# Performance work log

Measured on AMD Instinct MI355X. Metric: run time of the kernel, lower is better.

## Reference

```python
import math
import jax, jax.numpy as jnp
import numpy as np

NUM_HEADS = 16
LN_EPS = 1e-5


def setup_inputs() -> dict:
    key = jax.random.key(0)
    ks = jax.random.split(key, 8)
    B, S, D = 2, 1024, 1024
    L, H = 4, NUM_HEADS
    hd = D // H
    return {
        "x": jax.random.normal(ks[0], (B, S, D), jnp.float32),
        "past_k": jax.random.normal(ks[1], (L, B, H, S, hd), jnp.float32),
        "past_v": jax.random.normal(ks[2], (L, B, H, S, hd), jnp.float32),
        "past_q": jax.random.normal(ks[3], (L, B, H, S, hd), jnp.float32),
        "Wqkv": jax.random.normal(ks[4], (3 * D, D), jnp.float32) * 0.02,
        "bqkv": jnp.zeros((3 * D,), jnp.float32),
        "Wout": jax.random.normal(ks[5], (D, D), jnp.float32) * 0.02,
        "bout": jnp.zeros((D,), jnp.float32),
    }


def reference(x, past_k, past_v, past_q, Wqkv, bqkv, Wout, bout):
    B, S, D = x.shape
    H = NUM_HEADS
    hd = D // H
    scale = 1.0 / math.sqrt(hd)

    # qkv projection + head split: [B,S,D] -> [B,H,S,hd] each
    qkv = x @ Wqkv.T + bqkv  # [B,S,3D]
    q, k, v = jnp.split(qkv, 3, axis=-1)
    split = lambda t: t.reshape(B, S, H, hd).transpose(0, 2, 1, 3)
    q, k, v = split(q), split(k), split(v)

    # causal token attention scores [B,H,S,S]
    token_scores = jnp.einsum("bhqd,bhkd->bhqk", q, k) * scale
    causal = jnp.triu(jnp.ones((S, S), bool), k=1)
    token_scores = jnp.where(causal, -jnp.inf, token_scores)

    # stack past layers: [L,B,H,S,hd] -> [B,S,L,D]
    def to_full(t):
        L = t.shape[0]
        return t.transpose(1, 3, 0, 2, 4).reshape(B, S, L, D)

    mem = jnp.concatenate([to_full(past_q), to_full(past_k), to_full(past_v)], axis=2)  # [B,S,M,D], M=3L
    M = mem.shape[2]

    # layer norm (no affine) over feature dim
    mu = mem.mean(-1, keepdims=True)
    var = mem.var(-1, keepdims=True)
    mem = (mem - mu) / jnp.sqrt(var + LN_EPS)

    # reproject through K/V slices of qkv weight
    Wk, bk = Wqkv[D:2 * D], bqkv[D:2 * D]
    Wv, bv = Wqkv[2 * D:], bqkv[2 * D:]
    rk = (mem @ Wk.T + bk).reshape(B, S, M, H, hd).transpose(0, 3, 1, 2, 4)  # [B,H,S,M,hd]
    rv = (mem @ Wv.T + bv).reshape(B, S, M, H, hd).transpose(0, 3, 1, 2, 4)

    # memory scores via per-position elementwise reduce [B,H,S,M]
    mem_scores = jnp.einsum("bhsd,bhsmd->bhsm", q, rk) * scale

    scores = jnp.concatenate([token_scores, mem_scores], axis=-1)  # [B,H,S,S+M]
    weights = jax.nn.softmax(scores, axis=-1)
    token_w, mem_w = weights[..., :S], weights[..., S:]

    token_ctx = jnp.einsum("bhqk,bhkd->bhqd", token_w, v)
    mem_ctx = jnp.einsum("bhsm,bhsmd->bhsd", mem_w, rv)
    attn = token_ctx + mem_ctx  # [B,H,S,hd]

    merged = attn.transpose(0, 2, 1, 3).reshape(B, S, D)
    out = merged @ Wout.T + bout
    return out, (k, v, q)
```

## Files before the change

### kernel.cpp

```cpp
#include <hip/hip_runtime.h>

#define BATCH 2
#define SEQ   1024
#define DIM   1024
#define NH    16
#define HD    64
#define NM    12
#define NTOK  (BATCH*SEQ)
#define MEMROWS (BATCH*SEQ*NM)
#define OUTT  2097152
#define NEGBIG (-1.0e30f)

typedef __attribute__((ext_vector_type(8))) short short8;
typedef __attribute__((ext_vector_type(4))) float f32x4;

__device__ __forceinline__ float bf2f(ushort u) {
    union { unsigned int i; float f; } t; t.i = ((unsigned int)u) << 16; return t.f;
}
__device__ __forceinline__ ushort f2bf(float f) {
    union { float f; unsigned int i; } t; t.f = f;
    unsigned int i = t.i;
    unsigned int lsb = (i >> 16) & 1u;
    i += 0x7fffu + lsb;
    return (ushort)(i >> 16);
}

__global__ __launch_bounds__(256) void cvt3_kernel(
    const float* __restrict__ a, ushort* __restrict__ ab, int na4,
    const float* __restrict__ b, ushort* __restrict__ bb, int nb4,
    const float* __restrict__ c, ushort* __restrict__ cb, int nc4)
{
    int i = blockIdx.x * 256 + threadIdx.x;
    if (i >= na4 + nb4 + nc4) return;
    const float* src; ushort* dst; int j;
    if (i < na4)            { src = a; dst = ab; j = i; }
    else if (i < na4 + nb4) { src = b; dst = bb; j = i - na4; }
    else                    { src = c; dst = cb; j = i - na4 - nb4; }
    float4 v = ((const float4*)src)[j];
    ushort4 o; o.x = f2bf(v.x); o.y = f2bf(v.y); o.z = f2bf(v.z); o.w = f2bf(v.w);
    ((ushort4*)dst)[j] = o;
}


#define QKV_BLKS 384
__global__ __launch_bounds__(256) void qkv_ln_fused_kernel(
    const ushort* __restrict__ xb, const ushort* __restrict__ Wb,
    const float* __restrict__ bias, float* __restrict__ out,
    ushort* __restrict__ qkvb,
    const float* __restrict__ pq, const float* __restrict__ pk,
    const float* __restrict__ pv, ushort* __restrict__ mem_n)
{
    const int bid = blockIdx.x;
    const int tid = threadIdx.x;
    if (bid < QKV_BLKS) {
        __shared__ ushort As[128][40];
        __shared__ ushort Bs[128][40];
        const int w = tid >> 6, lane = tid & 63;
        const int n = lane & 15, qd = lane >> 4;
        const int wr = (w >> 1) * 64, wc = (w & 1) * 64;
        const int row0 = (bid / 24) * 128, col0 = (bid % 24) * 128;
        const int r1 = tid >> 2, o1 = (tid & 3) * 8;
        const int r2 = (tid + 256) >> 2, o2 = ((tid + 256) & 3) * 8;

        f32x4 acc[4][4];
#pragma unroll
        for (int mt = 0; mt < 4; mt++)
#pragma unroll
            for (int nt = 0; nt < 4; nt++) acc[mt][nt] = (f32x4){0.f, 0.f, 0.f, 0.f};

        for (int k0 = 0; k0 < 1024; k0 += 32) {
            *(short8*)&As[r1][o1] = *(const short8*)(xb + (size_t)(row0 + r1) * 1024 + k0 + o1);
            *(short8*)&As[r2][o2] = *(const short8*)(xb + (size_t)(row0 + r2) * 1024 + k0 + o2);
            *(short8*)&Bs[r1][o1] = *(const short8*)(Wb + (size_t)(col0 + r1) * 1024 + k0 + o1);
            *(short8*)&Bs[r2][o2] = *(const short8*)(Wb + (size_t)(col0 + r2) * 1024 + k0 + o2);
            __syncthreads();
            short8 af[4], bf[4];
#pragma unroll
            for (int mt = 0; mt < 4; mt++) af[mt] = *(const short8*)&As[wr + mt * 16 + n][qd * 8];
#pragma unroll
            for (int nt = 0; nt < 4; nt++) bf[nt] = *(const short8*)&Bs[wc + nt * 16 + n][qd * 8];
#pragma unroll
            for (int mt = 0; mt < 4; mt++)
#pragma unroll
                for (int nt = 0; nt < 4; nt++)
                    acc[mt][nt] = __builtin_amdgcn_mfma_f32_16x16x32_bf16(af[mt], bf[nt], acc[mt][nt], 0, 0, 0);
            __syncthreads();
        }
#pragma unroll
        for (int mt = 0; mt < 4; mt++)
#pragma unroll
            for (int nt = 0; nt < 4; nt++)
#pragma unroll
                for (int r = 0; r < 4; r++) {
                    int row = row0 + wr + mt * 16 + qd * 4 + r;
                    int col = col0 + wc + nt * 16 + n;
                    float val = acc[mt][nt][r] + bias[col];
                    int t = col >> 10, h = (col >> 6) & 15, d = col & 63;
                    int b = row >> 10, s = row & 1023;
                    size_t idx = (((size_t)(b * NH + h) * SEQ + s) * HD) + d;
                    size_t base = (t == 0) ? (size_t)3 * OUTT : (t == 1) ? (size_t)OUTT : (size_t)2 * OUTT;
                    out[base + idx] = val;
                    qkvb[(size_t)t * OUTT + idx] = f2bf(val);
                }
    } else {
        const int wid = tid >> 6, lane = tid & 63;
        const int r = (bid - QKV_BLKS) * 4 + wid;
        const int idx = r % NM;
        const int bs = r / NM;
        const int s = bs & (SEQ - 1);
        const int b = bs >> 10;
        const int c = idx >> 2;
        const int l = idx & 3;
        const float* src = (c == 0) ? pq : ((c == 1) ? pk : pv);
        const size_t base = ((size_t)(l * BATCH + b) * NH) * (SEQ * HD) + (size_t)s * HD;

        float4 v4[4];
        float sum = 0.f, sumsq = 0.f;
#pragma unroll
        for (int p = 0; p < 4; p++) {
            int h = p * 4 + (lane >> 4);
            int d = (lane & 15) * 4;
            float4 v = *(const float4*)(src + base + (size_t)h * (SEQ * HD) + d);
            v4[p] = v;
            sum   += v.x + v.y + v.z + v.w;
            sumsq += v.x * v.x + v.y * v.y + v.z * v.z + v.w * v.w;
        }
#pragma unroll
        for (int off = 32; off > 0; off >>= 1) {
            sum   += __shfl_xor(sum, off);
            sumsq += __shfl_xor(sumsq, off);
        }
        float mu  = sum * (1.f / 1024.f);
        float var = fmaxf(sumsq * (1.f / 1024.f) - mu * mu, 0.f);
        float inv = rsqrtf(var + 1e-5f);
        ushort* dst = mem_n + (size_t)r * 1024;
#pragma unroll
        for (int p = 0; p < 4; p++) {
            int dp = (p * 64 + lane) * 4;
            ushort4 o;
            o.x = f2bf((v4[p].x - mu) * inv);
            o.y = f2bf((v4[p].y - mu) * inv);
            o.z = f2bf((v4[p].z - mu) * inv);
            o.w = f2bf((v4[p].w - mu) * inv);
            *(ushort4*)(dst + dp) = o;
        }
    }
}

__global__ __launch_bounds__(256) void mfma_out_kernel(
    const ushort* __restrict__ Ab, const ushort* __restrict__ Wb,
    const float* __restrict__ bias, float* __restrict__ C)
{
    __shared__ ushort As[128][40];
    __shared__ ushort Bs[128][40];
    const int tid = threadIdx.x;
    const int w = tid >> 6, lane = tid & 63;
    const int n = lane & 15, qd = lane >> 4;
    const int wr = (w >> 1) * 64, wc = (w & 1) * 64;
    const int row0 = blockIdx.y * 128, col0 = blockIdx.x * 128;
    const int r1 = tid >> 2, o1 = (tid & 3) * 8;
    const int r2 = (tid + 256) >> 2, o2 = ((tid + 256) & 3) * 8;

    f32x4 acc[4][4];
#pragma unroll
    for (int mt = 0; mt < 4; mt++)
#pragma unroll
        for (int nt = 0; nt < 4; nt++) acc[mt][nt] = (f32x4){0.f, 0.f, 0.f, 0.f};

    for (int k0 = 0; k0 < 1024; k0 += 32) {
        *(short8*)&As[r1][o1] = *(const short8*)(Ab + (size_t)(row0 + r1) * 1024 + k0 + o1);
        *(short8*)&As[r2][o2] = *(const short8*)(Ab + (size_t)(row0 + r2) * 1024 + k0 + o2);
        *(short8*)&Bs[r1][o1] = *(const short8*)(Wb + (size_t)(col0 + r1) * 1024 + k0 + o1);
        *(short8*)&Bs[r2][o2] = *(const short8*)(Wb + (size_t)(col0 + r2) * 1024 + k0 + o2);
        __syncthreads();
        short8 af[4], bf[4];
#pragma unroll
        for (int mt = 0; mt < 4; mt++) af[mt] = *(const short8*)&As[wr + mt * 16 + n][qd * 8];
#pragma unroll
        for (int nt = 0; nt < 4; nt++) bf[nt] = *(const short8*)&Bs[wc + nt * 16 + n][qd * 8];
#pragma unroll
        for (int mt = 0; mt < 4; mt++)
#pragma unroll
            for (int nt = 0; nt < 4; nt++)
                acc[mt][nt] = __builtin_amdgcn_mfma_f32_16x16x32_bf16(af[mt], bf[nt], acc[mt][nt], 0, 0, 0);
        __syncthreads();
    }
#pragma unroll
    for (int mt = 0; mt < 4; mt++)
#pragma unroll
        for (int nt = 0; nt < 4; nt++)
#pragma unroll
            for (int r = 0; r < 4; r++) {
                int row = row0 + wr + mt * 16 + qd * 4 + r;
                int col = col0 + wc + nt * 16 + n;
                C[(size_t)row * 1024 + col] = acc[mt][nt][r] + bias[col];
            }
}

__global__ __launch_bounds__(256) void mfma_vproj_kernel(
    const ushort* __restrict__ wvecb, const ushort* __restrict__ Wvb,
    const float* __restrict__ bv, const float* __restrict__ wmem,
    ushort* __restrict__ mergedb)
{
    __shared__ ushort As[128][40];
    __shared__ ushort Bs[64][40];
    const int tid = threadIdx.x;
    const int w = tid >> 6, lane = tid & 63;
    const int n = lane & 15, qd = lane >> 4;
    const int wr = (w >> 1) * 64, wc = (w & 1) * 32;
    const int row0 = blockIdx.x * 128;
    const int h = blockIdx.y;
    const int r1 = tid >> 2, o1 = (tid & 3) * 8;
    const int r2 = (tid + 256) >> 2, o2 = ((tid + 256) & 3) * 8;

    f32x4 acc[4][2];
#pragma unroll
    for (int mt = 0; mt < 4; mt++)
#pragma unroll
        for (int nt = 0; nt < 2; nt++) acc[mt][nt] = (f32x4){0.f, 0.f, 0.f, 0.f};

    for (int k0 = 0; k0 < 1024; k0 += 32) {
        *(short8*)&As[r1][o1] = *(const short8*)(wvecb + ((size_t)(row0 + r1) * NH + h) * 1024 + k0 + o1);
        *(short8*)&As[r2][o2] = *(const short8*)(wvecb + ((size_t)(row0 + r2) * NH + h) * 1024 + k0 + o2);
        *(short8*)&Bs[r1 & 63][o1] = *(const short8*)(Wvb + (size_t)(h * HD + (r1 & 63)) * 1024 + k0 + o1);
        __syncthreads();
        short8 af[4], bf[2];
#pragma unroll
        for (int mt = 0; mt < 4; mt++) af[mt] = *(const short8*)&As[wr + mt * 16 + n][qd * 8];
#pragma unroll
        for (int nt = 0; nt < 2; nt++) bf[nt] = *(const short8*)&Bs[wc + nt * 16 + n][qd * 8];
#pragma unroll
        for (int mt = 0; mt < 4; mt++)
#pragma unroll
            for (int nt = 0; nt < 2; nt++)
                acc[mt][nt] = __builtin_amdgcn_mfma_f32_16x16x32_bf16(af[mt], bf[nt], acc[mt][nt], 0, 0, 0);
        __syncthreads();
    }
#pragma unroll
    for (int mt = 0; mt < 4; mt++)
#pragma unroll
        for (int nt = 0; nt < 2; nt++)
#pragma unroll
            for (int r = 0; r < 4; r++) {
                int token = row0 + wr + mt * 16 + qd * 4 + r;
                int d = wc + nt * 16 + n;
                float ws = wmem[((size_t)token * NH + h) * 16 + 12];
                size_t mi = (size_t)token * DIM + h * HD + d;
                float val = bf2f(mergedb[mi]) + acc[mt][nt][r] + ws * bv[h * HD + d];
                mergedb[mi] = f2bf(val);
            }
}

#define MSC_T 8
__global__ __launch_bounds__(256) void msc_direct_kernel(
    const ushort* __restrict__ qkvb, const ushort* __restrict__ mem_n,
    const ushort* __restrict__ Wkb, const float* __restrict__ bqkv,
    float* __restrict__ msc)
{
    __shared__ ushort qs[MSC_T][16][72];
    __shared__ ushort memc[MSC_T][12][72];
    __shared__ ushort qpc[MSC_T][16][72];
    __shared__ ushort wks[4][64][72];
    __shared__ float  qbkL[MSC_T][16];

    const int tid = threadIdx.x;
    const int w = tid >> 6, lane = tid & 63;
    const int n = lane & 15, qd = lane >> 4;
    const int t0 = blockIdx.x * MSC_T;

    {
        const int rid = tid >> 1, half = tid & 1;
        const int t = rid >> 4, h = rid & 15;
        const int g = t0 + t, b = g >> 10, s = g & 1023;
        const ushort* src = qkvb + (((size_t)(b * NH + h) * SEQ + s) * HD) + half * 32;
        *(short8*)&qs[t][h][half * 32]      = *(const short8*)(src);
        *(short8*)&qs[t][h][half * 32 + 8]  = *(const short8*)(src + 8);
        *(short8*)&qs[t][h][half * 32 + 16] = *(const short8*)(src + 16);
        *(short8*)&qs[t][h][half * 32 + 24] = *(const short8*)(src + 24);
    }
    __syncthreads();
    if (tid < 128) {
        const int t = tid >> 4, h = tid & 15;
        const float* bk = bqkv + DIM + h * HD;
        float s = 0.f;
#pragma unroll
        for (int d = 0; d < HD; d++) s += bf2f(qs[t][h][d]) * bk[d];
        qbkL[t][h] = s;
    }

    f32x4 acc[2];
    acc[0] = (f32x4){0.f, 0.f, 0.f, 0.f};
    acc[1] = (f32x4){0.f, 0.f, 0.f, 0.f};

    for (int ch = 0; ch < 16; ch++) {
        const int c0 = ch * 64;
        __syncthreads();
#pragma unroll
        for (int i = 0; i < 3; i++) {
            int sid = i * 256 + tid;
            int row = sid >> 3, o8 = (sid & 7) * 8;
            int t = row / 12, m = row % 12;
            *(short8*)&memc[t][m][o8] =
                *(const short8*)(mem_n + ((size_t)(t0 + t) * NM + m) * 1024 + c0 + o8);
        }
#pragma unroll
        for (int hh = 0; hh < 4; hh++) {
            const int h = w * 4 + hh;
            const ushort* wsrc = Wkb + (size_t)(h * HD + lane) * 1024 + c0;
#pragma unroll
            for (int j = 0; j < 4; j++) {
                ushort t16[16];
                *(short8*)&t16[0] = *(const short8*)(wsrc + j * 16);
                *(short8*)&t16[8] = *(const short8*)(wsrc + j * 16 + 8);
#pragma unroll
                for (int c = 0; c < 16; c++) wks[w][j * 16 + c][lane] = t16[c];
            }
            short8 af0 = *(const short8*)&qs[n & 7][h][qd * 8];
            short8 af1 = *(const short8*)&qs[n & 7][h][32 + qd * 8];
#pragma unroll
            for (int nt = 0; nt < 4; nt++) {
                short8 bf0 = *(const short8*)&wks[w][nt * 16 + n][qd * 8];
                short8 bf1 = *(const short8*)&wks[w][nt * 16 + n][32 + qd * 8];
                f32x4 z = (f32x4){0.f, 0.f, 0.f, 0.f};
                z = __builtin_amdgcn_mfma_f32_16x16x32_bf16(af0, bf0, z, 0, 0, 0);
                z = __builtin_amdgcn_mfma_f32_16x16x32_bf16(af1, bf1, z, 0, 0, 0);
                if (qd < 2) {
#pragma unroll
                    for (int r = 0; r < 4; r++)
                        qpc[qd * 4 + r][h][nt * 16 + n] = f2bf(z[r]);
                }
            }
        }
        __syncthreads();
#pragma unroll
        for (int p = 0; p < 2; p++) {
            const int tw = w + p * 4;
            const int mrow = (n < NM) ? n : 0;
            short8 af0 = *(const short8*)&qpc[tw][n][qd * 8];
            short8 af1 = *(const short8*)&qpc[tw][n][32 + qd * 8];
            short8 bf0 = *(const short8*)&memc[tw][mrow][qd * 8];
            short8 bf1 = *(const short8*)&memc[tw][mrow][32 + qd * 8];
            acc[p] = __builtin_amdgcn_mfma_f32_16x16x32_bf16(af0, bf0, acc[p], 0, 0, 0);
            acc[p] = __builtin_amdgcn_mfma_f32_16x16x32_bf16(af1, bf1, acc[p], 0, 0, 0);
        }
    }
    if (n < NM) {
#pragma unroll
        for (int p = 0; p < 2; p++) {
            const int tw = w + p * 4;
            const size_t gt = t0 + tw;
#pragma unroll
            for (int r = 0; r < 4; r++) {
                int h = qd * 4 + r;
                msc[(gt * NH + h) * NM + n] = 0.125f * (acc[p][r] + qbkL[tw][h]);
            }
        }
    }
}

#define TQ 64
#define TK 64
__global__ __launch_bounds__(512) void flash_attn_kernel(
    const ushort* __restrict__ qkvb, const float* __restrict__ msc,
    ushort* __restrict__ mergedb, float* __restrict__ wmem)
{
    __shared__ __align__(16) char smem[55296];
    ushort (*Ks)[TK][72]  = (ushort (*)[TK][72])smem;
    ushort (*Vt)[HD][72]  = (ushort (*)[HD][72])(smem + 18432);
    ushort (*Ps)[16][72]  = (ushort (*)[16][72])(smem + 36864);
    float  (*cbuf)[64][25] = (float (*)[64][25])smem;

    const int bxr = blockIdx.x;
    const int qt = (bxr & 1) ? (bxr >> 1) : (15 - (bxr >> 1));
    const int bh = blockIdx.y;
    const int b = bh >> 4, h = bh & 15;
    const int tid = threadIdx.x;
    const int w = tid >> 6;
    const int g = w >> 2;
    const int wq = w & 3;
    const int lane = tid & 63;
    const int n = lane & 15;
    const int qd = lane >> 4;

    const ushort* qb = qkvb;
    const ushort* kb = qkvb + (size_t)OUTT;
    const ushort* vb = qkvb + (size_t)2 * OUTT;
    const size_t headoff = (size_t)bh * SEQ * HD;

    const int qrow0 = qt * TQ + wq * 16;
    const ushort* qp = qb + headoff + (size_t)(qrow0 + n) * HD;
    short8 qf0 = *(const short8*)(qp + qd * 8);
    short8 qf1 = *(const short8*)(qp + 32 + qd * 8);

    float mrow[4], lrow[4];
    f32x4 Oacc[4];
#pragma unroll
    for (int r = 0; r < 4; r++) { mrow[r] = NEGBIG; lrow[r] = 0.f; }
#pragma unroll
    for (int nt = 0; nt < 4; nt++) Oacc[nt] = (f32x4){0.f, 0.f, 0.f, 0.f};

    const int gtid = tid & 255;
    const int key = gtid >> 2;
    const int c0 = (gtid & 3) * 16;
    const int nsteps = (qt + 2) >> 1;

    for (int step = 0; step < nsteps; ++step) {
        const int kt = 2 * step + g;
        const bool act = (kt <= qt);
        if (act) {
            const ushort* kg = kb + headoff + (size_t)(kt * TK + key) * HD + c0;
            *(short8*)&Ks[g][key][c0]     = *(const short8*)kg;
            *(short8*)&Ks[g][key][c0 + 8] = *(const short8*)(kg + 8);
            const ushort* vg = vb + headoff + (size_t)(kt * TK + key) * HD + c0;
            ushort vs[16];
            *(short8*)&vs[0] = *(const short8*)vg;
            *(short8*)&vs[8] = *(const short8*)(vg + 8);
#pragma unroll
            for (int i = 0; i < 16; i++) Vt[g][c0 + i][key] = vs[i];
        }
        __syncthreads();
        if (act) {
            f32x4 sacc[4];
#pragma unroll
            for (int kc = 0; kc < 4; kc++) {
                short8 kf0 = *(const short8*)&Ks[g][kc * 16 + n][qd * 8];
                short8 kf1 = *(const short8*)&Ks[g][kc * 16 + n][32 + qd * 8];
                f32x4 z = (f32x4){0.f, 0.f, 0.f, 0.f};
                z = __builtin_amdgcn_mfma_f32_16x16x32_bf16(qf0, kf0, z, 0, 0, 0);
                z = __builtin_amdgcn_mfma_f32_16x16x32_bf16(qf1, kf1, z, 0, 0, 0);
                sacc[kc] = z;
            }
            const bool diag = (kt == qt);
#pragma unroll
            for (int kc = 0; kc < 4; kc++) {
#pragma unroll
                for (int r = 0; r < 4; r++) {
                    float sv = sacc[kc][r] * 0.125f;
                    if (diag) {
                        int qrow = qrow0 + qd * 4 + r;
                        int kk = kt * TK + kc * 16 + n;
                        if (kk > qrow) sv = NEGBIG;
                    }
                    sacc[kc][r] = sv;
                }
            }
            float alpha[4];
#pragma unroll
            for (int r = 0; r < 4; r++) {
                float mx = fmaxf(fmaxf(sacc[0][r], sacc[1][r]), fmaxf(sacc[2][r], sacc[3][r]));
                mx = fmaxf(mx, __shfl_xor(mx, 1));
                mx = fmaxf(mx, __shfl_xor(mx, 2));
                mx = fmaxf(mx, __shfl_xor(mx, 4));
                mx = fmaxf(mx, __shfl_xor(mx, 8));
                float mnew = fmaxf(mrow[r], mx);
                alpha[r] = __expf(mrow[r] - mnew);
                mrow[r] = mnew;
            }
            float psum[4] = {0.f, 0.f, 0.f, 0.f};
#pragma unroll
            for (int kc = 0; kc < 4; kc++) {
#pragma unroll
                for (int r = 0; r < 4; r++) {
                    float p = __expf(sacc[kc][r] - mrow[r]);
                    psum[r] += p;
                    Ps[w][qd * 4 + r][kc * 16 + n] = f2bf(p);
                }
            }
#pragma unroll
            for (int r = 0; r < 4; r++) {
                float ps = psum[r];
                ps += __shfl_xor(ps, 1);
                ps += __shfl_xor(ps, 2);
                ps += __shfl_xor(ps, 4);
                ps += __shfl_xor(ps, 8);
                lrow[r] = alpha[r] * lrow[r] + ps;
            }
#pragma unroll
            for (int nt = 0; nt < 4; nt++)
#pragma unroll
                for (int r = 0; r < 4; r++)
                    Oacc[nt][r] *= alpha[r];
            short8 pf0 = *(const short8*)&Ps[w][n][qd * 8];
            short8 pf1 = *(const short8*)&Ps[w][n][32 + qd * 8];
#pragma unroll
            for (int nt = 0; nt < 4; nt++) {
                short8 vf0 = *(const short8*)&Vt[g][nt * 16 + n][qd * 8];
                short8 vf1 = *(const short8*)&Vt[g][nt * 16 + n][32 + qd * 8];
                f32x4 z = Oacc[nt];
                z = __builtin_amdgcn_mfma_f32_16x16x32_bf16(pf0, vf0, z, 0, 0, 0);
                z = __builtin_amdgcn_mfma_f32_16x16x32_bf16(pf1, vf1, z, 0, 0, 0);
                Oacc[nt] = z;
            }
        }
        __syncthreads();
    }

    if (g == 1) {
        float* cb = cbuf[wq][lane];
#pragma unroll
        for (int nt = 0; nt < 4; nt++)
#pragma unroll
            for (int r = 0; r < 4; r++) cb[nt * 4 + r] = Oacc[nt][r];
#pragma unroll
        for (int r = 0; r < 4; r++) { cb[16 + r] = mrow[r]; cb[20 + r] = lrow[r]; }
    }
    __syncthreads();
    if (g == 1) return;

    {
        const float* cb = cbuf[wq][lane];
#pragma unroll
        for (int r = 0; r < 4; r++) {
            float m1 = cb[16 + r], l1 = cb[20 + r];
            float mnew = fmaxf(mrow[r], m1);
            float a0 = __expf(mrow[r] - mnew);
            float a1 = __expf(m1 - mnew);
            lrow[r] = a0 * lrow[r] + a1 * l1;
#pragma unroll
            for (int nt = 0; nt < 4; nt++)
                Oacc[nt][r] = a0 * Oacc[nt][r] + a1 * cb[nt * 4 + r];
            mrow[r] = mnew;
        }
    }

#pragma unroll
    for (int r = 0; r < 4; r++) {
        int srow = qrow0 + qd * 4 + r;
        const float* mp = msc + ((size_t)(b * SEQ + srow) * NH + h) * NM;
        float mm = NEGBIG;
#pragma unroll
        for (int j = 0; j < NM; j++) mm = fmaxf(mm, mp[j]);
        float mf = fmaxf(mrow[r], mm);
        float al = __expf(mrow[r] - mf);
        float msum = 0.f;
#pragma unroll
        for (int j = 0; j < NM; j++) msum += __expf(mp[j] - mf);
        float lf = al * lrow[r] + msum;
        float inv = 1.f / lf;
        float scale = al * inv;
        ushort* mrow_out = mergedb + (size_t)(b * SEQ + srow) * DIM + h * HD;
#pragma unroll
        for (int nt = 0; nt < 4; nt++)
            mrow_out[nt * 16 + n] = f2bf(Oacc[nt][r] * scale);
        size_t wb = ((size_t)(b * SEQ + srow) * NH + h) * 16;
        if (n < 12)       wmem[wb + n]  = __expf(mp[n] - mf) * inv;
        else if (n == 12) wmem[wb + 12] = msum * inv;
    }
}

__global__ __launch_bounds__(256) void wvec_kernel(
    const float* __restrict__ wmem, const ushort* __restrict__ mem_n,
    ushort* __restrict__ wvecb)
{
    __shared__ ushort memL[NM][1032];
    __shared__ float wL[NH][NM];
    const int bs = blockIdx.x;
    const int tid = threadIdx.x;

    for (int t = tid; t < NM * 256; t += 256) {
        int m = t >> 8, c4 = (t & 255) << 2;
        *(ushort4*)&memL[m][c4] = *(const ushort4*)(mem_n + ((size_t)bs * NM + m) * 1024 + c4);
    }
    if (tid < NH * NM) {
        int h = tid / NM, m = tid % NM;
        wL[h][m] = wmem[((size_t)bs * NH + h) * 16 + m];
    }
    __syncthreads();

    for (int h = 0; h < NH; h++) {
#pragma unroll
        for (int c0 = 0; c0 < 1024; c0 += 256) {
            int c = c0 + tid;
            float acc = 0.f;
#pragma unroll
            for (int m = 0; m < NM; m++)
                acc = fmaf(wL[h][m], bf2f(memL[m][c]), acc);
            wvecb[((size_t)bs * NH + h) * 1024 + c] = f2bf(acc);
        }
    }
}

extern "C" void kernel_launch(void* const* d_in, const int* in_sizes, int n_in,
                              void* d_out, int out_size, void* d_ws, size_t ws_size,
                              hipStream_t stream) {
    const float* x    = (const float*)d_in[0];
    const float* pk   = (const float*)d_in[1];
    const float* pv   = (const float*)d_in[2];
    const float* pq   = (const float*)d_in[3];
    const float* Wqkv = (const float*)d_in[4];
    const float* bqkv = (const float*)d_in[5];
    const float* Wout = (const float*)d_in[6];
    const float* bout = (const float*)d_in[7];
    float* out = (float*)d_out;

    ushort* mem_n  = (ushort*)d_ws;
    ushort* wvecb  = mem_n + (size_t)MEMROWS * 1024;
    float*  msc    = (float*)(wvecb + (size_t)NTOK * NH * 1024);
    float*  wmem   = msc + (size_t)NTOK * NH * NM;
    ushort* qkvb   = (ushort*)(wmem + (size_t)NTOK * NH * 16);
    ushort* Wqkvb  = qkvb + (size_t)3 * OUTT;
    ushort* Woutb  = Wqkvb + (size_t)3072 * 1024;
    ushort* xb     = Woutb + (size_t)1024 * 1024;
    ushort* mergedb = xb;

    const int na4 = NTOK * DIM / 4, nb4 = 3 * DIM * DIM / 4, nc4 = DIM * DIM / 4;

    cvt3_kernel<<<(na4 + nb4 + nc4 + 255) / 256, 256, 0, stream>>>(
        x, xb, na4, Wqkv, Wqkvb, nb4, Wout, Woutb, nc4);
    qkv_ln_fused_kernel<<<QKV_BLKS + MEMROWS / 4, 256, 0, stream>>>(
        xb, Wqkvb, bqkv, out, qkvb, pq, pk, pv, mem_n);
    msc_direct_kernel<<<NTOK / MSC_T, 256, 0, stream>>>(
        qkvb, mem_n, Wqkvb + (size_t)DIM * DIM, bqkv, msc);
    flash_attn_kernel<<<dim3(16, 32), 512, 0, stream>>>(qkvb, msc, mergedb, wmem);
    wvec_kernel<<<NTOK, 256, 0, stream>>>(wmem, mem_n, wvecb);
    mfma_vproj_kernel<<<dim3(16, NH), 256, 0, stream>>>(
        wvecb, Wqkvb + (size_t)2 * DIM * DIM, bqkv + 2 * DIM, wmem, mergedb);
    mfma_out_kernel<<<dim3(8, 16), 256, 0, stream>>>(mergedb, Woutb, bout, out);
}
```

Measured before the change: 398.6 us.

## Split memory-score kernel over K halves and drop shared staging and block barriers

The memory-score kernel now runs a second grid dimension that splits the 1024-wide reduction into two halves, writing partial scores to two buffers that flash attention sums on read. Each wave keeps its own Q fragments in registers and its own per-wave qpc buffer, and reads mem_n straight from global memory. This removes the shared q/mem staging and the block-wide __syncthreads, so the waves work independently. In exchange it doubles the grid, reads mem_n redundantly per wave, and reuses the wvecb workspace as the second partial buffer before wvec_kernel overwrites it.

```diff
diff --git a/kernel.cpp b/kernel.cpp
--- a/kernel.cpp
+++ b/kernel.cpp
@@ -255,54 +255,52 @@
 __global__ __launch_bounds__(256) void msc_direct_kernel(
     const ushort* __restrict__ qkvb, const ushort* __restrict__ mem_n,
     const ushort* __restrict__ Wkb, const float* __restrict__ bqkv,
-    float* __restrict__ msc)
+    float* __restrict__ msc0, float* __restrict__ msc1)
 {
-    __shared__ ushort qs[MSC_T][16][72];
-    __shared__ ushort memc[MSC_T][12][72];
-    __shared__ ushort qpc[MSC_T][16][72];
     __shared__ ushort wks[4][64][72];
-    __shared__ float  qbkL[MSC_T][16];
+    __shared__ ushort qpc[4][MSC_T][4][72];
 
     const int tid = threadIdx.x;
     const int w = tid >> 6, lane = tid & 63;
     const int n = lane & 15, qd = lane >> 4;
     const int t0 = blockIdx.x * MSC_T;
-
+    const int kh = blockIdx.y;
+
+    short8 af0[4], af1[4];
     {
-        const int rid = tid >> 1, half = tid & 1;
-        const int t = rid >> 4, h = rid & 15;
-        const int g = t0 + t, b = g >> 10, s = g & 1023;
-        const ushort* src = qkvb + (((size_t)(b * NH + h) * SEQ + s) * HD) + half * 32;
-        *(short8*)&qs[t][h][half * 32]      = *(const short8*)(src);
-        *(short8*)&qs[t][h][half * 32 + 8]  = *(const short8*)(src + 8);
-        *(short8*)&qs[t][h][half * 32 + 16] = *(const short8*)(src + 16);
-        *(short8*)&qs[t][h][half * 32 + 24] = *(const short8*)(src + 24);
-    }
-    __syncthreads();
-    if (tid < 128) {
-        const int t = tid >> 4, h = tid & 15;
-        const float* bk = bqkv + DIM + h * HD;
-        float s = 0.f;
-#pragma unroll
-        for (int d = 0; d < HD; d++) s += bf2f(qs[t][h][d]) * bk[d];
-        qbkL[t][h] = s;
-    }
-
-    f32x4 acc[2];
-    acc[0] = (f32x4){0.f, 0.f, 0.f, 0.f};
-    acc[1] = (f32x4){0.f, 0.f, 0.f, 0.f};
-
-    for (int ch = 0; ch < 16; ch++) {
-        const int c0 = ch * 64;
-        __syncthreads();
-#pragma unroll
-        for (int i = 0; i < 3; i++) {
-            int sid = i * 256 + tid;
-            int row = sid >> 3, o8 = (sid & 7) * 8;
-            int t = row / 12, m = row % 12;
-            *(short8*)&memc[t][m][o8] =
-                *(const short8*)(mem_n + ((size_t)(t0 + t) * NM + m) * 1024 + c0 + o8);
-        }
+        const int g = t0 + (n & 7), b = g >> 10, s = g & 1023;
+#pragma unroll
+        for (int hh = 0; hh < 4; hh++) {
+            const int h = w * 4 + hh;
+            const ushort* qrow = qkvb + (((size_t)(b * NH + h) * SEQ + s) * HD);
+            af0[hh] = *(const short8*)(qrow + qd * 8);
+            af1[hh] = *(const short8*)(qrow + 32 + qd * 8);
+        }
+    }
+    float qbkv[4] = {0.f, 0.f, 0.f, 0.f};
+    if (kh == 0) {
+#pragma unroll
+        for (int hh = 0; hh < 4; hh++) {
+            const int h = w * 4 + hh;
+            const float* bk = bqkv + DIM + h * HD;
+            float s = 0.f;
+#pragma unroll
+            for (int j = 0; j < 8; j++) {
+                s += bf2f((ushort)af0[hh][j]) * bk[qd * 8 + j];
+                s += bf2f((ushort)af1[hh][j]) * bk[32 + qd * 8 + j];
+            }
+            s += __shfl_xor(s, 16);
+            s += __shfl_xor(s, 32);
+            qbkv[hh] = s;
+        }
+    }
+
+    f32x4 acc[MSC_T];
+#pragma unroll
+    for (int t = 0; t < MSC_T; t++) acc[t] = (f32x4){0.f, 0.f, 0.f, 0.f};
+
+    for (int ch = 0; ch < 8; ch++) {
+        const int c0 = (kh * 8 + ch) * 64;
 #pragma unroll
         for (int hh = 0; hh < 4; hh++) {
             const int h = w * 4 + hh;
@@ -315,44 +313,45 @@
 #pragma unroll
                 for (int c = 0; c < 16; c++) wks[w][j * 16 + c][lane] = t16[c];
             }
-            short8 af0 = *(const short8*)&qs[n & 7][h][qd * 8];
-            short8 af1 = *(const short8*)&qs[n & 7][h][32 + qd * 8];
 #pragma unroll
             for (int nt = 0; nt < 4; nt++) {
                 short8 bf0 = *(const short8*)&wks[w][nt * 16 + n][qd * 8];
                 short8 bf1 = *(const short8*)&wks[w][nt * 16 + n][32 + qd * 8];
                 f32x4 z = (f32x4){0.f, 0.f, 0.f, 0.f};
-                z = __builtin_amdgcn_mfma_f32_16x16x32_bf16(af0, bf0, z, 0, 0, 0);
-                z = __builtin_amdgcn_mfma_f32_16x16x32_bf16(af1, bf1, z, 0, 0, 0);
+                z = __builtin_amdgcn_mfma_f32_16x16x32_bf16(af0[hh], bf0, z, 0, 0, 0);
+                z = __builtin_amdgcn_mfma_f32_16x16x32_bf16(af1[hh], bf1, z, 0, 0, 0);
                 if (qd < 2) {
 #pragma unroll
                     for (int r = 0; r < 4; r++)
-                        qpc[qd * 4 + r][h][nt * 16 + n] = f2bf(z[r]);
+                        qpc[w][qd * 4 + r][hh][nt * 16 + n] = f2bf(z[r]);
                 }
             }
         }
-        __syncthreads();
-#pragma unroll
-        for (int p = 0; p < 2; p++) {
-            const int tw = w + p * 4;
+#pragma unroll
+        for (int t = 0; t < MSC_T; t++) {
+            const int g = t0 + t;
             const int mrow = (n < NM) ? n : 0;
-            short8 af0 = *(const short8*)&qpc[tw][n][qd * 8];
-            short8 af1 = *(const short8*)&qpc[tw][n][32 + qd * 8];
-            short8 bf0 = *(const short8*)&memc[tw][mrow][qd * 8];
-            short8 bf1 = *(const short8*)&memc[tw][mrow][32 + qd * 8];
-            acc[p] = __builtin_amdgcn_mfma_f32_16x16x32_bf16(af0, bf0, acc[p], 0, 0, 0);
-            acc[p] = __builtin_amdgcn_mfma_f32_16x16x32_bf16(af1, bf1, acc[p], 0, 0, 0);
-        }
-    }
-    if (n < NM) {
-#pragma unroll
-        for (int p = 0; p < 2; p++) {
-            const int tw = w + p * 4;
-            const size_t gt = t0 + tw;
-#pragma unroll
-            for (int r = 0; r < 4; r++) {
-                int h = qd * 4 + r;
-                msc[(gt * NH + h) * NM + n] = 0.125f * (acc[p][r] + qbkL[tw][h]);
+            const ushort* mb = mem_n + ((size_t)g * NM + mrow) * 1024 + c0;
+            short8 a0 = *(const short8*)&qpc[w][t][n & 3][qd * 8];
+            short8 a1 = *(const short8*)&qpc[w][t][n & 3][32 + qd * 8];
+            short8 b0 = *(const short8*)(mb + qd * 8);
+            short8 b1 = *(const short8*)(mb + 32 + qd * 8);
+            acc[t] = __builtin_amdgcn_mfma_f32_16x16x32_bf16(a0, b0, acc[t], 0, 0, 0);
+            acc[t] = __builtin_amdgcn_mfma_f32_16x16x32_bf16(a1, b1, acc[t], 0, 0, 0);
+        }
+    }
+#pragma unroll
+    for (int t = 0; t < MSC_T; t++) {
+        const size_t g = t0 + t;
+#pragma unroll
+        for (int r = 0; r < 4; r++) {
+            float qb = __shfl(qbkv[r], t);
+            if (qd == 0 && n < NM) {
+                const int h = w * 4 + r;
+                if (kh == 0)
+                    msc0[(g * NH + h) * NM + n] = 0.125f * (acc[t][r] + qb);
+                else
+                    msc1[(g * NH + h) * NM + n] = 0.125f * acc[t][r];
             }
         }
     }
@@ -361,7 +360,8 @@
 #define TQ 64
 #define TK 64
 __global__ __launch_bounds__(512) void flash_attn_kernel(
-    const ushort* __restrict__ qkvb, const float* __restrict__ msc,
+    const ushort* __restrict__ qkvb, const float* __restrict__ msc0,
+    const float* __restrict__ msc1,
     ushort* __restrict__ mergedb, float* __restrict__ wmem)
 {
     __shared__ __align__(16) char smem[55296];
@@ -526,15 +526,18 @@
 #pragma unroll
     for (int r = 0; r < 4; r++) {
         int srow = qrow0 + qd * 4 + r;
-        const float* mp = msc + ((size_t)(b * SEQ + srow) * NH + h) * NM;
+        const size_t midx = ((size_t)(b * SEQ + srow) * NH + h) * NM;
+        float mpv[NM];
+#pragma unroll
+        for (int j = 0; j < NM; j++) mpv[j] = msc0[midx + j] + msc1[midx + j];
         float mm = NEGBIG;
 #pragma unroll
-        for (int j = 0; j < NM; j++) mm = fmaxf(mm, mp[j]);
+        for (int j = 0; j < NM; j++) mm = fmaxf(mm, mpv[j]);
         float mf = fmaxf(mrow[r], mm);
         float al = __expf(mrow[r] - mf);
         float msum = 0.f;
 #pragma unroll
-        for (int j = 0; j < NM; j++) msum += __expf(mp[j] - mf);
+        for (int j = 0; j < NM; j++) msum += __expf(mpv[j] - mf);
         float lf = al * lrow[r] + msum;
         float inv = 1.f / lf;
         float scale = al * inv;
@@ -543,7 +546,7 @@
         for (int nt = 0; nt < 4; nt++)
             mrow_out[nt * 16 + n] = f2bf(Oacc[nt][r] * scale);
         size_t wb = ((size_t)(b * SEQ + srow) * NH + h) * 16;
-        if (n < 12)       wmem[wb + n]  = __expf(mp[n] - mf) * inv;
+        if (n < 12)       wmem[wb + n]  = __expf(mpv[n] - mf) * inv;
         else if (n == 12) wmem[wb + 12] = msum * inv;
     }
 }
@@ -602,6 +605,7 @@
     ushort* Woutb  = Wqkvb + (size_t)3072 * 1024;
     ushort* xb     = Woutb + (size_t)1024 * 1024;
     ushort* mergedb = xb;
+    float*  msc2   = (float*)wvecb;
 
     const int na4 = NTOK * DIM / 4, nb4 = 3 * DIM * DIM / 4, nc4 = DIM * DIM / 4;
 
@@ -609,9 +613,9 @@
         x, xb, na4, Wqkv, Wqkvb, nb4, Wout, Woutb, nc4);
     qkv_ln_fused_kernel<<<QKV_BLKS + MEMROWS / 4, 256, 0, stream>>>(
         xb, Wqkvb, bqkv, out, qkvb, pq, pk, pv, mem_n);
-    msc_direct_kernel<<<NTOK / MSC_T, 256, 0, stream>>>(
-        qkvb, mem_n, Wqkvb + (size_t)DIM * DIM, bqkv, msc);
-    flash_attn_kernel<<<dim3(16, 32), 512, 0, stream>>>(qkvb, msc, mergedb, wmem);
+    msc_direct_kernel<<<dim3(NTOK / MSC_T, 2), 256, 0, stream>>>(
+        qkvb, mem_n, Wqkvb + (size_t)DIM * DIM, bqkv, msc, msc2);
+    flash_attn_kernel<<<dim3(16, 32), 512, 0, stream>>>(qkvb, msc, msc2, mergedb, wmem);
     wvec_kernel<<<NTOK, 256, 0, stream>>>(wmem, mem_n, wvecb);
     mfma_vproj_kernel<<<dim3(16, NH), 256, 0, stream>>>(
         wvecb, Wqkvb + (size_t)2 * DIM * DIM, bqkv + 2 * DIM, wmem, mergedb);
```

Result: no change. 404.6 us (+1.5%).
